# Optimization experiments

Hardware: AMD Instinct MI355X
Metric: run time of the kernel (lower is better)

The kernel has to match this reference:

```python
import jax, jax.numpy as jnp
import numpy as np

N = 50000      # nodes
E = 800000     # edges (before self-loops)
HD = 256       # hidden_dim
H = 4          # heads
C = 64         # per-head channels (hidden_dim // 4)
L = 3          # num_layers
G = 512        # graphs in batch
NEG = 0.2      # LeakyReLU negative slope
EPS = 1e-5     # BatchNorm eps


def setup_inputs() -> dict:
    key = jax.random.key(0)
    ks = jax.random.split(key, 16)
    s_in = 1.0 / np.sqrt(HD)
    inp = {
        "x": jax.random.normal(ks[0], (N, 9), dtype=jnp.float32),
        "edge_index": jax.random.randint(ks[1], (2, E), 0, N, dtype=jnp.int64),
        "edge_attr": jax.random.normal(ks[2], (E, 5), dtype=jnp.float32),
        "batch": jnp.sort(jax.random.randint(ks[3], (N,), 0, G, dtype=jnp.int64)),
        # embeddings
        "Wn": jax.random.normal(ks[4], (9, HD), dtype=jnp.float32) / 3.0,
        "bn_b": jnp.zeros((HD,), jnp.float32),
        "We": jax.random.normal(ks[5], (5, HD), dtype=jnp.float32) / 2.3,
        "be_b": jnp.zeros((HD,), jnp.float32),
        # per-layer GATConv params (stacked over L)
        "lin_w": jax.random.normal(ks[6], (L, HD, H * C), dtype=jnp.float32) * s_in,
        "att_src": jax.random.normal(ks[7], (L, H, C), dtype=jnp.float32) * s_in,
        "att_dst": jax.random.normal(ks[8], (L, H, C), dtype=jnp.float32) * s_in,
        "lin_edge_w": jax.random.normal(ks[9], (L, HD, H * C), dtype=jnp.float32) * s_in,
        "att_edge": jax.random.normal(ks[10], (L, H, C), dtype=jnp.float32) * s_in,
        "conv_bias": jnp.zeros((L, H * C), jnp.float32),
        # BatchNorm affine params (eval mode: running_mean=0, running_var=1)
        "gamma": jnp.ones((L, HD), jnp.float32),
        "beta": jnp.zeros((L, HD), jnp.float32),
    }
    return inp


def _segment_softmax(logits, seg, num):
    m = jax.ops.segment_max(logits, seg, num_segments=num)
    m = jnp.where(jnp.isfinite(m), m, 0.0)
    e = jnp.exp(logits - m[seg])
    s = jax.ops.segment_sum(e, seg, num_segments=num)
    return e / (s[seg] + 1e-16)


def _gat_layer(x, row, col, edge_attr, lin_w, att_s, att_d, lin_e_w, att_e, bias):
    # add self-loops; self-loop edge_attr = mean of incoming edge_attr (PyG fill_value='mean')
    deg = jax.ops.segment_sum(jnp.ones((row.shape[0],), x.dtype), col, num_segments=N)
    loop_attr = jax.ops.segment_sum(edge_attr, col, num_segments=N) / jnp.maximum(deg, 1.0)[:, None]
    sl = jnp.arange(N, dtype=row.dtype)
    r = jnp.concatenate([row, sl])
    c = jnp.concatenate([col, sl])
    ea = jnp.concatenate([edge_attr, loop_attr], axis=0)  # [E+N, HD]

    xh = (x @ lin_w).reshape(N, H, C)                     # [N,H,C]
    a_src = jnp.einsum('nhc,hc->nh', xh, att_s)           # [N,H]
    a_dst = jnp.einsum('nhc,hc->nh', xh, att_d)
    eh = (ea @ lin_e_w).reshape(-1, H, C)                 # [E+N,H,C]
    a_e = jnp.einsum('ehc,hc->eh', eh, att_e)

    alpha = a_src[r] + a_dst[c] + a_e                     # [E+N,H]
    alpha = jnp.where(alpha >= 0, alpha, NEG * alpha)     # leaky_relu
    alpha = _segment_softmax(alpha, c, N)

    msg = xh[r] * alpha[:, :, None]                       # gather + weight
    out = jax.ops.segment_sum(msg, c, num_segments=N)     # scatter-add
    return out.reshape(N, H * C) + bias


def reference(x, edge_index, edge_attr, batch, Wn, bn_b, We, be_b,
              lin_w, att_src, att_dst, lin_edge_w, att_edge, conv_bias,
              gamma, beta):
    row, col = edge_index[0], edge_index[1]
    h = x @ Wn + bn_b                     # node embedding [N,HD]
    ea = edge_attr @ We + be_b            # edge embedding [E,HD]
    inv_std = 1.0 / jnp.sqrt(1.0 + EPS)   # BN eval, running stats (0,1)
    for l in range(L):
        h = _gat_layer(h, row, col, ea, lin_w[l], att_src[l], att_dst[l],
                       lin_edge_w[l], att_edge[l], conv_bias[l])
        h = h * inv_std * gamma[l] + beta[l]
        h = jax.nn.relu(h)                # dropout = identity (eval)
    # global mean pool over graphs
    cnt = jax.ops.segment_sum(jnp.ones((N,), h.dtype), batch, num_segments=G)
    pooled = jax.ops.segment_sum(h, batch, num_segments=G) / jnp.maximum(cnt, 1.0)[:, None]
    return pooled
```

## Files before the change

kernel.cpp:

```cpp
#include <hip/hip_runtime.h>
#include <hip/hip_fp16.h>
#include <math.h>

#define HD 256
#define NHEAD 4
#define CH 64
#define NLAYER 3
#define NEG_SLOPE 0.2f

typedef __attribute__((ext_vector_type(8))) _Float16 half8;
typedef __attribute__((ext_vector_type(4))) _Float16 half4v;
typedef __attribute__((ext_vector_type(4))) float float4v;
typedef __attribute__((ext_vector_type(4))) unsigned uint4v;

__global__ __launch_bounds__(256) void embed_count_kernel(
    const float* __restrict__ x, const float* __restrict__ Wn,
    const float* __restrict__ bn_b, _Float16* __restrict__ h, int N,
    const int* __restrict__ col, int* __restrict__ deg, int E,
    int embedBlocks) {
  int tid = threadIdx.x;
  if ((int)blockIdx.x < embedBlocks) {
    int base = blockIdx.x * 8;
    __shared__ float xs[8][9];
    int nn = N - base;
    if (nn > 8) nn = 8;
    if (tid < nn * 9) xs[tid / 9][tid % 9] = x[(size_t)base * 9 + tid];
    __syncthreads();
    float b = bn_b[tid];
    for (int i = 0; i < nn; ++i) {
      float v = b;
#pragma unroll
      for (int k = 0; k < 9; ++k) v += xs[i][k] * Wn[k * HD + tid];
      h[(size_t)(base + i) * HD + tid] = (_Float16)v;
    }
  } else {
    int e = (blockIdx.x - embedBlocks) * 256 + tid;
    if (e < E) atomicAdd(&deg[col[e]], 1);
  }
}

__global__ __launch_bounds__(256) void wc_bfrag_kernel(
    const float* __restrict__ lin_edge_w, const float* __restrict__ att_edge,
    const float* __restrict__ We, const float* __restrict__ be_b,
    float* __restrict__ Wc, float* __restrict__ bc,
    const float* __restrict__ lin_w, _Float16* __restrict__ Bf_hi) {
  int tid = threadIdx.x;
  if (blockIdx.x < 12) {
    int lh = blockIdx.x;
    int l = lh >> 2, hh = lh & 3;
    __shared__ float weff[256];
    int j = tid;
    const float* lw = lin_edge_w + (size_t)l * HD * HD + (size_t)j * HD + hh * CH;
    const float* ae = att_edge + l * HD + hh * CH;
    float s = 0.f;
#pragma unroll 8
    for (int c = 0; c < CH; ++c) s += lw[c] * ae[c];
    weff[j] = s;
    __syncthreads();
    if (j < 5) {
      float acc = 0.f;
      for (int t = 0; t < 256; ++t) acc += We[j * HD + t] * weff[t];
      Wc[j * 12 + lh] = acc;
    } else if (j == 5) {
      float acc = 0.f;
      for (int t = 0; t < 256; ++t) acc += be_b[t] * weff[t];
      bc[lh] = acc;
    }
  } else {
    int bid = (blockIdx.x - 12) * 4 + (tid >> 6);
    int l = bid >> 7;
    int kt = (bid >> 4) & 7, ntg = bid & 15;
    int lane = tid & 63;
    const float* B = lin_w + (size_t)l * HD * HD;
    size_t base = ((size_t)bid * 64 + lane) * 8;
    int k0 = kt * 32 + (lane >> 4) * 8;
    int n = ((ntg >= 8) ? 128 : 0) + (lane & 15) * 8 + (ntg & 7);
#pragma unroll
    for (int j = 0; j < 8; ++j) {
      Bf_hi[base + j] = (_Float16)B[(size_t)(k0 + j) * HD + n];
    }
  }
}

__global__ __launch_bounds__(256) void tile_sums_kernel(
    const int* __restrict__ deg, int* __restrict__ tsum, int N) {
  __shared__ int red[256];
  int i = blockIdx.x * 256 + threadIdx.x;
  red[threadIdx.x] = (i < N) ? deg[i] : 0;
  __syncthreads();
  for (int off = 128; off > 0; off >>= 1) {
    if (threadIdx.x < off) red[threadIdx.x] += red[threadIdx.x + off];
    __syncthreads();
  }
  if (threadIdx.x == 0) tsum[blockIdx.x] = red[0];
}

__global__ __launch_bounds__(64) void scan_tsums_kernel(
    const int* __restrict__ tsum, int* __restrict__ toff, int T) {
  int lane = threadIdx.x;
  int carry = 0;
  for (int base = 0; base < T; base += 64) {
    int i = base + lane;
    int orig = (i < T) ? tsum[i] : 0;
    int v = orig;
#pragma unroll
    for (int off = 1; off < 64; off <<= 1) {
      int t = __shfl_up(v, off, 64);
      if (lane >= off) v += t;
    }
    if (i < T) toff[i] = carry + v - orig;
    carry += __shfl(v, 63, 64);
  }
}

__global__ __launch_bounds__(256) void scan_local_kernel(
    const int* __restrict__ deg, const int* __restrict__ toff,
    int* __restrict__ row_start, int N, int E) {
  __shared__ int buf[256];
  int i = blockIdx.x * 256 + threadIdx.x;
  int v = (i < N) ? deg[i] : 0;
  buf[threadIdx.x] = v;
  __syncthreads();
  for (int off = 1; off < 256; off <<= 1) {
    int t = (threadIdx.x >= off) ? buf[threadIdx.x - off] : 0;
    __syncthreads();
    buf[threadIdx.x] += t;
    __syncthreads();
  }
  if (i < N) row_start[i] = toff[blockIdx.x] + buf[threadIdx.x] - v;
  if (blockIdx.x == 0 && threadIdx.x == 0) row_start[N] = E;
}

__global__ __launch_bounds__(256) void scatter_csr_ae_kernel(
    const int* __restrict__ row, const int* __restrict__ col,
    const float* __restrict__ edge_attr, const int* __restrict__ row_start,
    int* __restrict__ cursor, const float* __restrict__ Wc,
    const float* __restrict__ bc, unsigned* __restrict__ ecsr, int E) {
  __shared__ float sWc[60];
  __shared__ float sbc[12];
  int t = threadIdx.x;
  if (t < 60) sWc[t] = Wc[t];
  if (t < 12) sbc[t] = bc[t];
  __syncthreads();
  int e = blockIdx.x * 256 + t;
  if (e >= E) return;
  int c = col[e];
  int p = atomicAdd(&cursor[c], 1);
  float ea[5];
#pragma unroll
  for (int k = 0; k < 5; ++k) ea[k] = edge_attr[(size_t)e * 5 + k];
  unsigned rec[8];
  rec[0] = (unsigned)row[e];
#pragma unroll
  for (int l = 0; l < NLAYER; ++l) {
    float av[NHEAD];
#pragma unroll
    for (int hh = 0; hh < NHEAD; ++hh) {
      int lh = l * NHEAD + hh;
      float s = sbc[lh];
#pragma unroll
      for (int k = 0; k < 5; ++k) s += ea[k] * sWc[k * 12 + lh];
      av[hh] = s;
    }
    __half2 p0 = __floats2half2_rn(av[0], av[1]);
    __half2 p1 = __floats2half2_rn(av[2], av[3]);
    rec[1 + 2 * l] = *(unsigned*)&p0;
    rec[2 + 2 * l] = *(unsigned*)&p1;
  }
  rec[7] = 0u;
  int slot = row_start[c] + p;
  uint4v* dst = (uint4v*)(ecsr + (size_t)slot * 8);
  uint4v v0 = {rec[0], rec[1], rec[2], rec[3]};
  uint4v v1 = {rec[4], rec[5], rec[6], rec[7]};
  dst[0] = v0;
  dst[1] = v1;
}

__global__ __launch_bounds__(512) void mfma_gemm_fused_kernel(
    const _Float16* __restrict__ A, const _Float16* __restrict__ Bf_hi,
    const float* __restrict__ att_s, const float* __restrict__ att_d,
    __half* __restrict__ xh_h, float* __restrict__ a_src,
    float* __restrict__ a_dst, int N) {
  __shared__ _Float16 sBh[4096];
  const int tid = threadIdx.x;
  const int wave = tid >> 6, lane = tid & 63;
  const int m = lane & 15, quad = lane >> 4;
  const int y = blockIdx.y;
  const int rowbase = blockIdx.x * 128 + wave * 16;
  const int arow = rowbase + m;
  const int arowc = (arow < N) ? arow : (N - 1);

  float4v acc[8];
#pragma unroll
  for (int nt = 0; nt < 8; ++nt) acc[nt] = (float4v){0.f, 0.f, 0.f, 0.f};

  for (int kt = 0; kt < 8; ++kt) {
    __syncthreads();
    {
      const float4* gh = (const float4*)(Bf_hi + ((size_t)kt * 16 + y * 8) * 512);
      ((float4*)sBh)[tid] = gh[tid];
    }
    half8 a = *(const half8*)(A + (size_t)arowc * HD + kt * 32 + quad * 8);
    __syncthreads();
#pragma unroll
    for (int nt = 0; nt < 8; ++nt) {
      half8 bhi = *(const half8*)&sBh[nt * 512 + lane * 8];
      acc[nt] = __builtin_amdgcn_mfma_f32_16x16x32_f16(a, bhi, acc[nt], 0, 0, 0);
    }
  }

  const int hh = y * 2 + (m >> 3);
  const int colbase = y * 128 + m * 8;
  float ats[8], atd[8];
#pragma unroll
  for (int nt = 0; nt < 8; ++nt) {
    ats[nt] = att_s[colbase + nt];
    atd[nt] = att_d[colbase + nt];
  }
  _Float16* xf = (_Float16*)xh_h;
#pragma unroll
  for (int r = 0; r < 4; ++r) {
    int orow = rowbase + quad * 4 + r;
    bool valid = orow < N;
    float ps = 0.f, pd = 0.f;
    half8 h0;
#pragma unroll
    for (int nt = 0; nt < 8; ++nt) {
      h0[nt] = (_Float16)acc[nt][r];
      ps += acc[nt][r] * ats[nt];
      pd += acc[nt][r] * atd[nt];
    }
    if (valid) {
      *(half8*)(xf + (size_t)orow * HD + colbase) = h0;
    }
    ps += __shfl_xor(ps, 1, 64);
    ps += __shfl_xor(ps, 2, 64);
    ps += __shfl_xor(ps, 4, 64);
    pd += __shfl_xor(pd, 1, 64);
    pd += __shfl_xor(pd, 2, 64);
    pd += __shfl_xor(pd, 4, 64);
    if (valid && (m & 7) == 0) {
      a_src[(size_t)orow * NHEAD + hh] = ps;
      a_dst[(size_t)orow * NHEAD + hh] = pd;
    }
  }
}

__global__ __launch_bounds__(256) void fused_aggregate_kernel(
    const __half* __restrict__ xh_h, const unsigned* __restrict__ ecsr,
    const int* __restrict__ row_start, int lsel,
    const float* __restrict__ a_src, const float* __restrict__ a_dst,
    const float* __restrict__ cb, const float* __restrict__ gm,
    const float* __restrict__ bt, float inv_std, _Float16* __restrict__ hout,
    int N) {
  const int tid = threadIdx.x;
  const int lane = tid & 63;
  const int hw = lane >> 4;
  const int eidx = lane & 15;
  const int t = lane;
  const int ch = t * 4;
  const char* __restrict__ xb = (const char*)xh_h;
  const char* __restrict__ eb = (const char*)ecsr;
  const char* __restrict__ ab = (const char*)a_src;
  const int aofs = 1 + 2 * lsel + (hw >> 1);
  const bool hi_half = (hw & 1);
  const int base_src = lane & 48;

  const float gs0 = gm[ch + 0] * inv_std, gs1 = gm[ch + 1] * inv_std;
  const float gs2 = gm[ch + 2] * inv_std, gs3 = gm[ch + 3] * inv_std;
  const float of0 = cb[ch + 0] * gs0 + bt[ch + 0];
  const float of1 = cb[ch + 1] * gs1 + bt[ch + 1];
  const float of2 = cb[ch + 2] * gs2 + bt[ch + 2];
  const float of3 = cb[ch + 3] * gs3 + bt[ch + 3];

  const int stride = gridDim.x * 4;
  for (int n = blockIdx.x * 4 + (tid >> 6); n < N; n += stride) {
    int s = row_start[n], e = row_start[n + 1];
    half4v sv = *(const half4v*)(xb + ((unsigned)n << 9) + ((unsigned)t << 3));
    float based = a_dst[(size_t)n * 4 + hw];

    float a0 = 0.f, a1 = 0.f, a2 = 0.f, a3 = 0.f;
    float zpart = 0.f, aepart = 0.f;

    for (int chunk = s; chunk < e; chunk += 16) {
      int myedge = chunk + eidx;
      bool mev = myedge < e;
      int r_my = 0;
      unsigned aw_u = 0;
      if (mev) {
        const unsigned* rp = (const unsigned*)(eb + ((unsigned)myedge << 5));
        r_my = (int)rp[0];
        aw_u = rp[aofs];
      }
      int ru[16];
#pragma unroll
      for (int u = 0; u < 16; ++u) ru[u] = __shfl(r_my, base_src + u, 64);
      half4v xv[16];
#pragma unroll
      for (int u = 0; u < 16; ++u)
        xv[u] = *(const half4v*)(xb + ((unsigned)ru[u] << 9) + ((unsigned)t << 3));

      float w_my = 0.f, ae = 0.f;
      if (mev) {
        __half2 h2 = *(__half2*)&aw_u;
        ae = hi_half ? __high2float(h2) : __low2float(h2);
        float lg = *(const float*)(ab + ((unsigned)r_my << 4) + ((unsigned)hw << 2))
                   + based + ae;
        lg = (lg >= 0.f) ? lg : NEG_SLOPE * lg;
        w_my = __expf(lg);
      }
      zpart += w_my;
      aepart += ae;

#pragma unroll
      for (int u = 0; u < 16; ++u) {
        float w = __shfl(w_my, base_src + u, 64);
        a0 += w * (float)xv[u][0];
        a1 += w * (float)xv[u][1];
        a2 += w * (float)xv[u][2];
        a3 += w * (float)xv[u][3];
      }
    }
#pragma unroll
    for (int off = 1; off < 16; off <<= 1) {
      zpart += __shfl_xor(zpart, off, 64);
      aepart += __shfl_xor(aepart, off, 64);
    }
    float dinv = (e > s) ? 1.0f / (float)(e - s) : 1.0f;
    float sl = *(const float*)(ab + ((unsigned)n << 4) + ((unsigned)hw << 2))
               + based + aepart * dinv;
    sl = (sl >= 0.f) ? sl : NEG_SLOPE * sl;
    float wself = __expf(sl);
    a0 += wself * (float)sv[0];
    a1 += wself * (float)sv[1];
    a2 += wself * (float)sv[2];
    a3 += wself * (float)sv[3];
    float zinv = 1.0f / (zpart + wself + 1e-16f);

    half4v ho;
    ho[0] = (_Float16)fmaxf(a0 * zinv * gs0 + of0, 0.f);
    ho[1] = (_Float16)fmaxf(a1 * zinv * gs1 + of1, 0.f);
    ho[2] = (_Float16)fmaxf(a2 * zinv * gs2 + of2, 0.f);
    ho[3] = (_Float16)fmaxf(a3 * zinv * gs3 + of3, 0.f);
    *(half4v*)&hout[(size_t)n * HD + ch] = ho;
  }
}

__global__ __launch_bounds__(128) void pool_kernel(
    const _Float16* __restrict__ h, const int* __restrict__ batch,
    float* __restrict__ out, int N) {
  int g = blockIdx.x;
  int tid = threadIdx.x;
  __shared__ int s_lo, s_hi;
  if (tid == 0) {
    int lo = 0, hi = N;
    while (lo < hi) { int mid = (lo + hi) >> 1; if (batch[mid] < g) lo = mid + 1; else hi = mid; }
    s_lo = lo;
    lo = 0; hi = N;
    while (lo < hi) { int mid = (lo + hi) >> 1; if (batch[mid] < g + 1) lo = mid + 1; else hi = mid; }
    s_hi = lo;
  }
  __syncthreads();
  int lo = s_lo, hi = s_hi;
  const __half2* h2 = (const __half2*)h;
  float a0 = 0.f, b0 = 0.f, a1 = 0.f, b1 = 0.f;
  float a2 = 0.f, b2 = 0.f, a3 = 0.f, b3 = 0.f;
  int n = lo;
  for (; n + 4 <= hi; n += 4) {
    __half2 v0 = h2[(size_t)(n + 0) * 128 + tid];
    __half2 v1 = h2[(size_t)(n + 1) * 128 + tid];
    __half2 v2 = h2[(size_t)(n + 2) * 128 + tid];
    __half2 v3 = h2[(size_t)(n + 3) * 128 + tid];
    a0 += __low2float(v0); b0 += __high2float(v0);
    a1 += __low2float(v1); b1 += __high2float(v1);
    a2 += __low2float(v2); b2 += __high2float(v2);
    a3 += __low2float(v3); b3 += __high2float(v3);
  }
  for (; n < hi; ++n) {
    __half2 v = h2[(size_t)n * 128 + tid];
    a0 += __low2float(v); b0 += __high2float(v);
  }
  float sa = (a0 + a1) + (a2 + a3);
  float sb = (b0 + b1) + (b2 + b3);
  int cnt = hi - lo;
  float inv = 1.0f / (float)(cnt > 0 ? cnt : 1);
  float2 o;
  o.x = sa * inv;
  o.y = sb * inv;
  *(float2*)&out[(size_t)g * HD + tid * 2] = o;
}

extern "C" void kernel_launch(void* const* d_in, const int* in_sizes, int n_in,
                              void* d_out, int out_size, void* d_ws, size_t ws_size,
                              hipStream_t stream) {
  const float* x = (const float*)d_in[0];
  const int* ei = (const int*)d_in[1];
  const float* edge_attr = (const float*)d_in[2];
  const int* batch = (const int*)d_in[3];
  const float* Wn = (const float*)d_in[4];
  const float* bn_b = (const float*)d_in[5];
  const float* We = (const float*)d_in[6];
  const float* be_b = (const float*)d_in[7];
  const float* lin_w = (const float*)d_in[8];
  const float* att_src = (const float*)d_in[9];
  const float* att_dst = (const float*)d_in[10];
  const float* lin_edge_w = (const float*)d_in[11];
  const float* att_edge = (const float*)d_in[12];
  const float* conv_bias = (const float*)d_in[13];
  const float* gamma = (const float*)d_in[14];
  const float* beta = (const float*)d_in[15];

  const int N = in_sizes[3];
  const int E = in_sizes[1] / 2;
  const int G = out_size / HD;
  const int* row = ei;
  const int* col = ei + E;

  char* ws = (char*)d_ws;
  size_t off = 0;
  auto alloc = [&](size_t bytes) -> char* {
    char* p = ws + off;
    off += (bytes + 255) & ~(size_t)255;
    return p;
  };
  _Float16* h = (_Float16*)alloc((size_t)N * HD * 2);
  __half* xh_h = (__half*)alloc((size_t)N * HD * 2);
  float* a_src = (float*)alloc((size_t)N * NHEAD * 4);
  float* a_dst = (float*)alloc((size_t)N * NHEAD * 4);
  unsigned* ecsr = (unsigned*)alloc((size_t)E * 32);
  int* deg = (int*)alloc((size_t)N * 4);
  int* row_start = (int*)alloc((size_t)(N + 1) * 4);
  int* cursor = (int*)alloc((size_t)N * 4);
  int* tsum = (int*)alloc(4096);
  int* toff = (int*)alloc(4096);
  float* Wc = (float*)alloc(64 * 4);
  float* bc = (float*)alloc(16 * 4);
  _Float16* Bf_hi = (_Float16*)alloc((size_t)NLAYER * HD * HD * 2);

  (void)hipMemsetAsync(deg, 0, (size_t)N * 4, stream);
  (void)hipMemsetAsync(cursor, 0, (size_t)N * 4, stream);

  int embedBlocks = (N + 7) / 8;
  int countBlocks = (E + 255) / 256;
  embed_count_kernel<<<embedBlocks + countBlocks, 256, 0, stream>>>(
      x, Wn, bn_b, h, N, col, deg, E, embedBlocks);
  wc_bfrag_kernel<<<12 + NLAYER * 32, 256, 0, stream>>>(
      lin_edge_w, att_edge, We, be_b, Wc, bc, lin_w, Bf_hi);
  int T = (N + 255) / 256;
  tile_sums_kernel<<<T, 256, 0, stream>>>(deg, tsum, N);
  scan_tsums_kernel<<<1, 64, 0, stream>>>(tsum, toff, T);
  scan_local_kernel<<<T, 256, 0, stream>>>(deg, toff, row_start, N, E);
  scatter_csr_ae_kernel<<<(E + 255) / 256, 256, 0, stream>>>(
      row, col, edge_attr, row_start, cursor, Wc, bc, ecsr, E);

  const float inv_std = 1.0f / sqrtf(1.0f + 1e-5f);
  int quads = (N + 3) / 4;
  int aggBlocks = quads < 2560 ? quads : 2560;
  for (int l = 0; l < NLAYER; ++l) {
    dim3 gg((N + 127) / 128, 2);
    mfma_gemm_fused_kernel<<<gg, 512, 0, stream>>>(
        h, Bf_hi + (size_t)l * HD * HD,
        att_src + l * HD, att_dst + l * HD, xh_h, a_src, a_dst, N);
    fused_aggregate_kernel<<<aggBlocks, 256, 0, stream>>>(
        xh_h, ecsr, row_start, l, a_src, a_dst,
        conv_bias + l * HD, gamma + l * HD, beta + l * HD, inv_std, h, N);
  }
  pool_kernel<<<G, 128, 0, stream>>>(h, batch, (float*)d_out, N);
}
```

Baseline: 489.7 us.

## Process two nodes per wavefront with 16-byte gathers and non-persistent grid

The aggregation kernel now maps two destination nodes to each 64-lane wave, with 32 lanes per node each handling 8 fp16 channels loaded as one 16-byte vector. Edges are processed in chunks of 8 instead of 16. The persistent grid-stride loop is replaced by one node pair per wave and a grid of N/8 blocks. The aim is wider memory transactions, fewer wasted lanes on low-degree nodes and better load balance, at the cost of more blocks and more accumulator registers per lane.

```diff
diff --git a/kernel.cpp b/kernel.cpp
--- a/kernel.cpp
+++ b/kernel.cpp
@@ -255,94 +255,97 @@
     int N) {
   const int tid = threadIdx.x;
   const int lane = tid & 63;
-  const int hw = lane >> 4;
-  const int eidx = lane & 15;
-  const int t = lane;
-  const int ch = t * 4;
+  const int wave = tid >> 6;
+  const int halfw = lane >> 5;
+  const int l32 = lane & 31;
+  const int hw = l32 >> 3;
+  const int eu = l32 & 7;
+  const int chb = l32 * 8;
   const char* __restrict__ xb = (const char*)xh_h;
   const char* __restrict__ eb = (const char*)ecsr;
   const char* __restrict__ ab = (const char*)a_src;
   const int aofs = 1 + 2 * lsel + (hw >> 1);
   const bool hi_half = (hw & 1);
-  const int base_src = lane & 48;
-
-  const float gs0 = gm[ch + 0] * inv_std, gs1 = gm[ch + 1] * inv_std;
-  const float gs2 = gm[ch + 2] * inv_std, gs3 = gm[ch + 3] * inv_std;
-  const float of0 = cb[ch + 0] * gs0 + bt[ch + 0];
-  const float of1 = cb[ch + 1] * gs1 + bt[ch + 1];
-  const float of2 = cb[ch + 2] * gs2 + bt[ch + 2];
-  const float of3 = cb[ch + 3] * gs3 + bt[ch + 3];
-
-  const int stride = gridDim.x * 4;
-  for (int n = blockIdx.x * 4 + (tid >> 6); n < N; n += stride) {
-    int s = row_start[n], e = row_start[n + 1];
-    half4v sv = *(const half4v*)(xb + ((unsigned)n << 9) + ((unsigned)t << 3));
-    float based = a_dst[(size_t)n * 4 + hw];
-
-    float a0 = 0.f, a1 = 0.f, a2 = 0.f, a3 = 0.f;
-    float zpart = 0.f, aepart = 0.f;
-
-    for (int chunk = s; chunk < e; chunk += 16) {
-      int myedge = chunk + eidx;
-      bool mev = myedge < e;
-      int r_my = 0;
-      unsigned aw_u = 0;
-      if (mev) {
-        const unsigned* rp = (const unsigned*)(eb + ((unsigned)myedge << 5));
-        r_my = (int)rp[0];
-        aw_u = rp[aofs];
-      }
-      int ru[16];
-#pragma unroll
-      for (int u = 0; u < 16; ++u) ru[u] = __shfl(r_my, base_src + u, 64);
-      half4v xv[16];
-#pragma unroll
-      for (int u = 0; u < 16; ++u)
-        xv[u] = *(const half4v*)(xb + ((unsigned)ru[u] << 9) + ((unsigned)t << 3));
-
-      float w_my = 0.f, ae = 0.f;
-      if (mev) {
-        __half2 h2 = *(__half2*)&aw_u;
-        ae = hi_half ? __high2float(h2) : __low2float(h2);
-        float lg = *(const float*)(ab + ((unsigned)r_my << 4) + ((unsigned)hw << 2))
-                   + based + ae;
-        lg = (lg >= 0.f) ? lg : NEG_SLOPE * lg;
-        w_my = __expf(lg);
-      }
-      zpart += w_my;
-      aepart += ae;
-
-#pragma unroll
-      for (int u = 0; u < 16; ++u) {
-        float w = __shfl(w_my, base_src + u, 64);
-        a0 += w * (float)xv[u][0];
-        a1 += w * (float)xv[u][1];
-        a2 += w * (float)xv[u][2];
-        a3 += w * (float)xv[u][3];
-      }
-    }
-#pragma unroll
-    for (int off = 1; off < 16; off <<= 1) {
-      zpart += __shfl_xor(zpart, off, 64);
-      aepart += __shfl_xor(aepart, off, 64);
-    }
-    float dinv = (e > s) ? 1.0f / (float)(e - s) : 1.0f;
-    float sl = *(const float*)(ab + ((unsigned)n << 4) + ((unsigned)hw << 2))
-               + based + aepart * dinv;
-    sl = (sl >= 0.f) ? sl : NEG_SLOPE * sl;
-    float wself = __expf(sl);
-    a0 += wself * (float)sv[0];
-    a1 += wself * (float)sv[1];
-    a2 += wself * (float)sv[2];
-    a3 += wself * (float)sv[3];
-    float zinv = 1.0f / (zpart + wself + 1e-16f);
-
-    half4v ho;
-    ho[0] = (_Float16)fmaxf(a0 * zinv * gs0 + of0, 0.f);
-    ho[1] = (_Float16)fmaxf(a1 * zinv * gs1 + of1, 0.f);
-    ho[2] = (_Float16)fmaxf(a2 * zinv * gs2 + of2, 0.f);
-    ho[3] = (_Float16)fmaxf(a3 * zinv * gs3 + of3, 0.f);
-    *(half4v*)&hout[(size_t)n * HD + ch] = ho;
+  const int bsrc = lane & 32;
+  const int bw = lane & 56;
+
+  int n = blockIdx.x * 8 + wave * 2 + halfw;
+  bool valid = n < N;
+  int nc = valid ? n : (N - 1);
+
+  int s = row_start[nc];
+  int e = row_start[nc + 1];
+  if (!valid) e = s;
+
+  half8 sv = *(const half8*)(xb + ((unsigned)nc << 9) + ((unsigned)l32 << 4));
+  float based = a_dst[(size_t)nc * 4 + hw];
+
+  float acc[8];
+#pragma unroll
+  for (int k = 0; k < 8; ++k) acc[k] = 0.f;
+  float zpart = 0.f, aepart = 0.f;
+
+  for (int chunk = s; chunk < e; chunk += 8) {
+    int myedge = chunk + eu;
+    bool mev = myedge < e;
+    unsigned r_w = 0, aw = 0;
+    if (mev) {
+      const unsigned* rp = (const unsigned*)(eb + ((size_t)(unsigned)myedge << 5));
+      r_w = rp[0];
+      aw = rp[aofs];
+    }
+    unsigned ru[8];
+#pragma unroll
+    for (int u = 0; u < 8; ++u) ru[u] = (unsigned)__shfl((int)r_w, bsrc + u, 64);
+    half8 xr[8];
+#pragma unroll
+    for (int u = 0; u < 8; ++u)
+      xr[u] = *(const half8*)(xb + (size_t)((ru[u] << 9) + ((unsigned)l32 << 4)));
+
+    float w_my = 0.f, ae = 0.f;
+    if (mev) {
+      __half2 h2 = *(__half2*)&aw;
+      ae = hi_half ? __high2float(h2) : __low2float(h2);
+      float lg = *(const float*)(ab + ((unsigned)r_w << 4) + ((unsigned)hw << 2))
+                 + based + ae;
+      lg = (lg >= 0.f) ? lg : NEG_SLOPE * lg;
+      w_my = __expf(lg);
+    }
+    zpart += w_my;
+    aepart += ae;
+
+#pragma unroll
+    for (int u = 0; u < 8; ++u) {
+      float w = __shfl(w_my, bw + u, 64);
+#pragma unroll
+      for (int k = 0; k < 8; ++k) acc[k] += w * (float)xr[u][k];
+    }
+  }
+  zpart += __shfl_xor(zpart, 1, 64);
+  zpart += __shfl_xor(zpart, 2, 64);
+  zpart += __shfl_xor(zpart, 4, 64);
+  aepart += __shfl_xor(aepart, 1, 64);
+  aepart += __shfl_xor(aepart, 2, 64);
+  aepart += __shfl_xor(aepart, 4, 64);
+
+  float dinv = (e > s) ? 1.0f / (float)(e - s) : 1.0f;
+  float sl = *(const float*)(ab + ((unsigned)nc << 4) + ((unsigned)hw << 2))
+             + based + aepart * dinv;
+  sl = (sl >= 0.f) ? sl : NEG_SLOPE * sl;
+  float wself = __expf(sl);
+#pragma unroll
+  for (int k = 0; k < 8; ++k) acc[k] += wself * (float)sv[k];
+  float zinv = 1.0f / (zpart + wself + 1e-16f);
+
+  if (valid) {
+    half8 ho;
+#pragma unroll
+    for (int k = 0; k < 8; ++k) {
+      float gsk = gm[chb + k] * inv_std;
+      float ofk = cb[chb + k] * gsk + bt[chb + k];
+      ho[k] = (_Float16)fmaxf(acc[k] * zinv * gsk + ofk, 0.f);
+    }
+    *(half8*)&hout[(size_t)n * HD + chb] = ho;
   }
 }
 
@@ -454,14 +457,12 @@
       row, col, edge_attr, row_start, cursor, Wc, bc, ecsr, E);
 
   const float inv_std = 1.0f / sqrtf(1.0f + 1e-5f);
-  int quads = (N + 3) / 4;
-  int aggBlocks = quads < 2560 ? quads : 2560;
   for (int l = 0; l < NLAYER; ++l) {
     dim3 gg((N + 127) / 128, 2);
     mfma_gemm_fused_kernel<<<gg, 512, 0, stream>>>(
         h, Bf_hi + (size_t)l * HD * HD,
         att_src + l * HD, att_dst + l * HD, xh_h, a_src, a_dst, N);
-    fused_aggregate_kernel<<<aggBlocks, 256, 0, stream>>>(
+    fused_aggregate_kernel<<<(N + 7) / 8, 256, 0, stream>>>(
         xh_h, ecsr, row_start, l, a_src, a_dst,
         conv_bias + l * HD, gamma + l * HD, beta + l * HD, inv_std, h, N);
   }
```

Result: faster. 476.3 us (-2.7%).
